# Kernel optimization log

Hardware: AMD Instinct MI355X
Metric: run time of the kernel (lower is better)

The kernel has to match this reference:

```python
import jax, jax.numpy as jnp
import numpy as np

B, D, E, C = 16384, 2048, 16, 64  # batch, feat_dim, num_experts, classes per expert
CLASS_STARTS = np.arange(E, dtype=np.int32) * C  # contiguous equal-size class ranges


def setup_inputs() -> dict:
    key = jax.random.key(0)
    k1, k2, k3, k4, k5 = jax.random.split(key, 5)
    return {
        "features": jax.random.normal(k1, (B, D), dtype=jnp.float32),
        "coarse_w": jax.random.normal(k2, (E, D), dtype=jnp.float32) * 0.02,
        "coarse_b": jax.random.normal(k3, (E,), dtype=jnp.float32) * 0.02,
        "expert_w": jax.random.normal(k4, (E, C, D), dtype=jnp.float32) * 0.02,
        "expert_b": jax.random.normal(k5, (E, C), dtype=jnp.float32) * 0.02,
    }


def reference(features, coarse_w, coarse_b, expert_w, expert_b):
    # coarse router: Linear(feat_dim -> num_experts)
    coarse_output = features @ coarse_w.T + coarse_b          # [B, E]
    expert_id = jnp.argmax(coarse_output, axis=1)             # [B] top-1 routing

    # all-expert heads as one batched GEMM, then select routed expert per sample
    # (same math as gather-by-mask + per-expert Linear + scatter-back loop)
    y_all = jnp.einsum('bd,ecd->bec', features, expert_w) + expert_b  # [B, E, C]
    y = jnp.take_along_axis(y_all, expert_id[:, None, None], axis=1)[:, 0, :]  # [B, C]

    # local_preds: softmax probs of the routed expert (all experts have C = max classes)
    local_preds = jax.nn.softmax(y, axis=1)                   # [B, C]

    # global prediction = local argmax + expert's class-range start
    starts = jnp.asarray(CLASS_STARTS)
    global_preds = (jnp.argmax(y, axis=1) + starts[expert_id]).astype(jnp.float32)  # [B]

    return coarse_output, expert_id, local_preds, global_preds
```

## Files before the change

### kernel.cpp

```cpp
#include <hip/hip_runtime.h>
#include <cstdint>

typedef _Float16 f16;
typedef f16 f16x8 __attribute__((ext_vector_type(8)));
typedef float f32x4 __attribute__((ext_vector_type(4)));
#define MFMA16(a, b, c) __builtin_amdgcn_mfma_f32_16x16x32_f16((a), (b), (c), 0, 0, 0)

static constexpr int B_ = 16384;
static constexpr int D_ = 2048;
static constexpr int E_ = 16;
static constexpr int C_ = 64;
static constexpr float LSC = 2048.0f;
static constexpr float ILSC = 1.0f / 2048.0f;
static constexpr int TR_E = 128;
static constexpr int SK_E = 8;
static constexpr int MAXITEMS = (B_ / TR_E) + E_;

__device__ __forceinline__ void cvt_hl(const float4 x, const float4 y,
                                       f16x8& h, f16x8& l) {
  const float av[8] = {x.x, x.y, x.z, x.w, y.x, y.y, y.z, y.w};
#pragma unroll
  for (int j = 0; j < 8; ++j) {
    const f16 hh = (f16)av[j];
    h[j] = hh;
    l[j] = (f16)((av[j] - (float)hh) * LSC);
  }
}

__global__ __launch_bounds__(256) void convert_w(
    const float* __restrict__ cw, const float* __restrict__ ew,
    f16* __restrict__ cwH, f16* __restrict__ cwL,
    f16* __restrict__ ewH, f16* __restrict__ ewL) {
  const int g = blockIdx.x;
  const int tid = threadIdx.x;
  const float* src;
  f16 *dh, *dl;
  size_t off;
  if (g < 16) {
    off = ((size_t)g * 256 + tid) * 8;
    src = cw; dh = cwH; dl = cwL;
  } else {
    off = ((size_t)(g - 16) * 256 + tid) * 8;
    src = ew; dh = ewH; dl = ewL;
  }
  const float4 v0 = *(const float4*)(src + off);
  const float4 v1 = *(const float4*)(src + off + 4);
  f16x8 h8, l8;
  cvt_hl(v0, v1, h8, l8);
  *(f16x8*)(dh + off) = h8;
  *(f16x8*)(dl + off) = l8;
}

__global__ __launch_bounds__(512) void coarse_fused(
    const float* __restrict__ feat, const f16* __restrict__ cwH,
    const f16* __restrict__ cwL, const float* __restrict__ cb,
    float* __restrict__ out0, float* __restrict__ out1,
    int* __restrict__ eidArr) {
  __shared__ float red[8 * 256];
  const int tid = threadIdx.x;
  const int w = tid >> 6;
  const int lane = tid & 63;
  const int rl = lane & 15;
  const int kq = lane >> 4;
  const int row = blockIdx.x * 16 + rl;
  const int k0 = w * (D_ / 8);

  const float* fr = feat + (size_t)row * D_ + k0 + kq * 8;
  const f16* bhp = cwH + (size_t)rl * D_ + k0 + kq * 8;
  const f16* blp = cwL + (size_t)rl * D_ + k0 + kq * 8;

  f32x4 aH = {0.f, 0.f, 0.f, 0.f};
  f32x4 aC = {0.f, 0.f, 0.f, 0.f};

  float4 v0 = *(const float4*)(fr);
  float4 v1 = *(const float4*)(fr + 4);
  f16x8 bhn = *(const f16x8*)(bhp);
  f16x8 bln = *(const f16x8*)(blp);
#pragma unroll
  for (int ch = 0; ch < 8; ++ch) {
    const float4 c0 = v0, c1 = v1;
    const f16x8 bh = bhn, bl = bln;
    if (ch + 1 < 8) {
      const int ko = (ch + 1) * 32;
      v0 = *(const float4*)(fr + ko);
      v1 = *(const float4*)(fr + ko + 4);
      bhn = *(const f16x8*)(bhp + ko);
      bln = *(const f16x8*)(blp + ko);
    }
    f16x8 h8, l8;
    cvt_hl(c0, c1, h8, l8);
    aH = MFMA16(h8, bh, aH);
    aC = MFMA16(h8, bl, aC);
    aC = MFMA16(l8, bh, aC);
  }
#pragma unroll
  for (int reg = 0; reg < 4; ++reg)
    red[w * 256 + (kq * 4 + reg) * 16 + rl] = aH[reg] + aC[reg] * ILSC;
  __syncthreads();

  if (tid < 256) {
    const int e = tid & 15;
    const int lrow = tid >> 4;
    float val = cb[e];
#pragma unroll
    for (int ww = 0; ww < 8; ++ww) val += red[ww * 256 + tid];
    const int grow = blockIdx.x * 16 + lrow;
    out0[(size_t)grow * E_ + e] = val;
    float av2 = val;
    int ai = e;
#pragma unroll
    for (int off = 8; off; off >>= 1) {
      const float ov = __shfl_xor(av2, off, 16);
      const int oi = __shfl_xor(ai, off, 16);
      if (ov > av2 || (ov == av2 && oi < ai)) { av2 = ov; ai = oi; }
    }
    if (e == 0) {
      out1[grow] = (float)ai;
      eidArr[grow] = ai;
    }
  }
}

__global__ __launch_bounds__(256) void route_build(
    const int* __restrict__ eidArr, int* __restrict__ cnt,
    int* __restrict__ rowList, int* __restrict__ sched,
    int* __restrict__ nItems, int* __restrict__ doneCnt) {
  __shared__ int lcnt[E_];
  __shared__ int lbase[E_];
  __shared__ int tiles[E_];
  __shared__ int offs[E_];
  __shared__ int isLast;
  const int tid = threadIdx.x;
  if (tid < E_) lcnt[tid] = 0;
  __syncthreads();
  const int row = blockIdx.x * 256 + tid;
  const int best = eidArr[row];
  const int lpos = atomicAdd(&lcnt[best], 1);
  __syncthreads();
  if (tid < E_) lbase[tid] = atomicAdd(&cnt[tid], lcnt[tid]);
  __syncthreads();
  rowList[best * B_ + lbase[best] + lpos] = row;

  __syncthreads();
  if (tid == 0) {
    __threadfence();
    const int d = atomicAdd(doneCnt, 1);
    isLast = (d == (int)gridDim.x - 1) ? 1 : 0;
  }
  __syncthreads();
  if (isLast) {
    if (tid < E_)
      tiles[tid] = (atomicAdd(&cnt[tid], 0) + TR_E - 1) / TR_E;
    __syncthreads();
    if (tid == 0) {
      int acc = 0;
      for (int e2 = 0; e2 < E_; ++e2) { offs[e2] = acc; acc += tiles[e2]; }
      *nItems = acc;
    }
    __syncthreads();
    if (tid < E_) {
      const int o = offs[tid], n = tiles[tid];
      for (int k = 0; k < n; ++k) sched[o + k] = tid | (k << 8);
    }
  }
}

__global__ __launch_bounds__(256) void expert_gemm(
    const float* __restrict__ feat,
    const f16* __restrict__ ewH, const f16* __restrict__ ewL,
    const int* __restrict__ rowList, const int* __restrict__ cnt,
    const int* __restrict__ sched, const int* __restrict__ nItems,
    float* __restrict__ part0, float* __restrict__ partRest) {
  __shared__ int rIdx[TR_E];
  const int b = blockIdx.x;
  const int kz = b % SK_E;
  const int item = b / SK_E;
  if (item >= *nItems) return;
  const int s = sched[item];
  const int e = s & 255;
  const int tile = s >> 8;
  const int count = cnt[e];

  const int tid = threadIdx.x;
  if (tid < TR_E) {
    const int slot = tile * TR_E + tid;
    rIdx[tid] = (slot < count) ? rowList[e * B_ + slot] : 0;
  }
  __syncthreads();

  const int lane = tid & 63;
  const int w = tid >> 6;
  const int rl = lane & 15;
  const int kq = lane >> 4;

  const int grow0 = rIdx[w * 32 + rl];
  const int grow1 = rIdx[w * 32 + 16 + rl];
  constexpr int KRANGE = D_ / SK_E;
  constexpr int NCH = KRANGE / 32;
  const int k0 = kz * KRANGE;

  const float* pa0 = feat + (size_t)grow0 * D_ + k0 + kq * 8;
  const float* pa1 = feat + (size_t)grow1 * D_ + k0 + kq * 8;
  const size_t eoff = (size_t)e * C_ * D_;
  const f16* pbh[4];
  const f16* pbl[4];
#pragma unroll
  for (int ct = 0; ct < 4; ++ct) {
    const size_t co = eoff + (size_t)(ct * 16 + rl) * D_ + k0 + kq * 8;
    pbh[ct] = ewH + co;
    pbl[ct] = ewL + co;
  }

  f32x4 accH[2][4], accC[2][4];
#pragma unroll
  for (int s2 = 0; s2 < 2; ++s2)
#pragma unroll
    for (int ct = 0; ct < 4; ++ct) {
      accH[s2][ct] = (f32x4){0.f, 0.f, 0.f, 0.f};
      accC[s2][ct] = (f32x4){0.f, 0.f, 0.f, 0.f};
    }

  float4 n0a = *(const float4*)(pa0);
  float4 n0b = *(const float4*)(pa0 + 4);
  float4 n1a = *(const float4*)(pa1);
  float4 n1b = *(const float4*)(pa1 + 4);
  f16x8 bhn[4], bln[4];
#pragma unroll
  for (int ct = 0; ct < 4; ++ct) {
    bhn[ct] = *(const f16x8*)(pbh[ct]);
    bln[ct] = *(const f16x8*)(pbl[ct]);
  }
#pragma unroll
  for (int ch = 0; ch < NCH; ++ch) {
    const float4 c0a = n0a, c0b = n0b, c1a = n1a, c1b = n1b;
    f16x8 bhc[4], blc[4];
#pragma unroll
    for (int ct = 0; ct < 4; ++ct) { bhc[ct] = bhn[ct]; blc[ct] = bln[ct]; }
    if (ch + 1 < NCH) {
      const int kn = (ch + 1) * 32;
      n0a = *(const float4*)(pa0 + kn);
      n0b = *(const float4*)(pa0 + kn + 4);
      n1a = *(const float4*)(pa1 + kn);
      n1b = *(const float4*)(pa1 + kn + 4);
#pragma unroll
      for (int ct = 0; ct < 4; ++ct) {
        bhn[ct] = *(const f16x8*)(pbh[ct] + kn);
        bln[ct] = *(const f16x8*)(pbl[ct] + kn);
      }
    }
    f16x8 a0h, a0l, a1h, a1l;
    cvt_hl(c0a, c0b, a0h, a0l);
    cvt_hl(c1a, c1b, a1h, a1l);
#pragma unroll
    for (int ct = 0; ct < 4; ++ct) {
      accH[0][ct] = MFMA16(a0h, bhc[ct], accH[0][ct]);
      accC[0][ct] = MFMA16(a0h, blc[ct], accC[0][ct]);
      accC[0][ct] = MFMA16(a0l, bhc[ct], accC[0][ct]);
      accH[1][ct] = MFMA16(a1h, bhc[ct], accH[1][ct]);
      accC[1][ct] = MFMA16(a1h, blc[ct], accC[1][ct]);
      accC[1][ct] = MFMA16(a1l, bhc[ct], accC[1][ct]);
    }
  }

  float* pk = kz ? (partRest + (size_t)(kz - 1) * B_ * C_) : part0;
#pragma unroll
  for (int s2 = 0; s2 < 2; ++s2)
#pragma unroll
    for (int reg = 0; reg < 4; ++reg) {
      const int rloc = w * 32 + s2 * 16 + kq * 4 + reg;
      const int slot = tile * TR_E + rloc;
      if (slot < count) {
        const int g = rIdx[rloc];
#pragma unroll
        for (int ct = 0; ct < 4; ++ct)
          pk[(size_t)g * C_ + ct * 16 + rl] =
              accH[s2][ct][reg] + accC[s2][ct][reg] * ILSC;
      }
    }
}

template <int SK>
__global__ __launch_bounds__(256) void finish_rows(
    const float* __restrict__ ypart0, const float* __restrict__ ypartRest,
    const float* __restrict__ eb, const int* __restrict__ eidArr,
    float* __restrict__ out2, float* __restrict__ out3) {
  const int lane = threadIdx.x & 63;
  const int row = (blockIdx.x * 256 + threadIdx.x) >> 6;
  const int eid = eidArr[row];

  float v = eb[eid * C_ + lane];
  v += ypart0[(size_t)row * C_ + lane];
#pragma unroll
  for (int kz = 1; kz < SK; ++kz)
    v += ypartRest[((size_t)(kz - 1) * B_ + row) * C_ + lane];

  float m = v;
#pragma unroll
  for (int off = 32; off; off >>= 1) m = fmaxf(m, __shfl_xor(m, off, 64));
  const float p = __expf(v - m);
  float s = p;
#pragma unroll
  for (int off = 32; off; off >>= 1) s += __shfl_xor(s, off, 64);
  out2[(size_t)row * C_ + lane] = p / s;

  float av = v;
  int ai = lane;
#pragma unroll
  for (int off = 32; off; off >>= 1) {
    const float ov = __shfl_xor(av, off, 64);
    const int oi = __shfl_xor(ai, off, 64);
    if (ov > av || (ov == av && oi < ai)) { av = ov; ai = oi; }
  }
  if (lane == 0) out3[row] = (float)(ai + (eid << 6));
}

extern "C" void kernel_launch(void* const* d_in, const int* in_sizes, int n_in,
                              void* d_out, int out_size, void* d_ws,
                              size_t ws_size, hipStream_t stream) {
  const float* feat = (const float*)d_in[0];
  const float* cw = (const float*)d_in[1];
  const float* cb = (const float*)d_in[2];
  const float* ew = (const float*)d_in[3];
  const float* eb = (const float*)d_in[4];

  float* out0 = (float*)d_out;
  float* out1 = out0 + (size_t)B_ * E_;
  float* out2 = out1 + B_;
  float* out3 = out2 + (size_t)B_ * C_;

  char* p = (char*)d_ws;
  f16* ewH = (f16*)p;        p += (size_t)E_ * C_ * D_ * 2;
  f16* ewL = (f16*)p;        p += (size_t)E_ * C_ * D_ * 2;
  f16* cwH = (f16*)p;        p += (size_t)E_ * D_ * 2;
  f16* cwL = (f16*)p;        p += (size_t)E_ * D_ * 2;
  float* ypartRest = (float*)p; p += (size_t)(SK_E - 1) * B_ * C_ * 4;
  int* rowList = (int*)p;    p += (size_t)E_ * B_ * 4;
  int* cnt = (int*)p;        p += 64 * 4;
  int* eidArr = (int*)p;     p += (size_t)B_ * 4;
  int* sched = (int*)p;      p += 512 * 4;
  int* nItems = (int*)p;
  int* doneCnt = cnt + 16;

  hipMemsetAsync(cnt, 0, 32 * sizeof(int), stream);

  convert_w<<<16 + 1024, 256, 0, stream>>>(cw, ew, cwH, cwL, ewH, ewL);
  coarse_fused<<<B_ / 16, 512, 0, stream>>>(feat, cwH, cwL, cb, out0, out1,
                                            eidArr);
  route_build<<<B_ / 256, 256, 0, stream>>>(eidArr, cnt, rowList, sched,
                                            nItems, doneCnt);
  expert_gemm<<<MAXITEMS * SK_E, 256, 0, stream>>>(
      feat, ewH, ewL, rowList, cnt, sched, nItems, out2, ypartRest);
  finish_rows<SK_E><<<(B_ * 64) / 256, 256, 0, stream>>>(out2, ypartRest, eb,
                                                         eidArr, out2, out3);
}
```

Baseline: 290.1 us.

## Fuse routing into coarse kernel and softmax epilogue into expert GEMM

Routing-list construction moves into the coarse kernel, so the separate route_build launch and the eidArr round trip go away. The counter memset is folded into the weight-conversion kernel. The expert GEMM changes from 128-row tiles with 8-way split-K partials to 16-row tiles with a 2-wave in-block K split. Bias, softmax and argmax now run in its epilogue, which removes the partial-sum buffers and the finish kernel. The trade-off is that each feature row and weight chunk is now reused far less per block, so weight traffic per output rises, and the blocks are small.

```diff
diff --git a/kernel.cpp b/kernel.cpp
--- a/kernel.cpp
+++ b/kernel.cpp
@@ -12,9 +12,8 @@
 static constexpr int C_ = 64;
 static constexpr float LSC = 2048.0f;
 static constexpr float ILSC = 1.0f / 2048.0f;
-static constexpr int TR_E = 128;
-static constexpr int SK_E = 8;
-static constexpr int MAXITEMS = (B_ / TR_E) + E_;
+static constexpr int TR_X = 16;
+static constexpr int MAXITEMS = B_ / TR_X + E_;
 
 __device__ __forceinline__ void cvt_hl(const float4 x, const float4 y,
                                        f16x8& h, f16x8& l) {
@@ -30,9 +29,10 @@
 __global__ __launch_bounds__(256) void convert_w(
     const float* __restrict__ cw, const float* __restrict__ ew,
     f16* __restrict__ cwH, f16* __restrict__ cwL,
-    f16* __restrict__ ewH, f16* __restrict__ ewL) {
+    f16* __restrict__ ewH, f16* __restrict__ ewL, int* __restrict__ cnt) {
   const int g = blockIdx.x;
   const int tid = threadIdx.x;
+  if (g == 0 && tid < 32) cnt[tid] = 0;
   const float* src;
   f16 *dh, *dl;
   size_t off;
@@ -55,13 +55,21 @@
     const float* __restrict__ feat, const f16* __restrict__ cwH,
     const f16* __restrict__ cwL, const float* __restrict__ cb,
     float* __restrict__ out0, float* __restrict__ out1,
-    int* __restrict__ eidArr) {
+    int* __restrict__ cnt, int* __restrict__ rowList,
+    int* __restrict__ sched, int* __restrict__ nItems,
+    int* __restrict__ doneCnt) {
   __shared__ float red[8 * 256];
+  __shared__ int lcnt[E_];
+  __shared__ int lbase[E_];
+  __shared__ int tiles[E_];
+  __shared__ int offs[E_];
+  __shared__ int isLast;
   const int tid = threadIdx.x;
   const int w = tid >> 6;
   const int lane = tid & 63;
   const int rl = lane & 15;
   const int kq = lane >> 4;
+  if (tid < E_) lcnt[tid] = 0;
   const int row = blockIdx.x * 16 + rl;
   const int k0 = w * (D_ / 8);
 
@@ -98,13 +106,14 @@
     red[w * 256 + (kq * 4 + reg) * 16 + rl] = aH[reg] + aC[reg] * ILSC;
   __syncthreads();
 
+  int best = -1, lpos = 0, grow = 0;
   if (tid < 256) {
     const int e = tid & 15;
     const int lrow = tid >> 4;
     float val = cb[e];
 #pragma unroll
     for (int ww = 0; ww < 8; ++ww) val += red[ww * 256 + tid];
-    const int grow = blockIdx.x * 16 + lrow;
+    grow = blockIdx.x * 16 + lrow;
     out0[(size_t)grow * E_ + e] = val;
     float av2 = val;
     int ai = e;
@@ -116,30 +125,14 @@
     }
     if (e == 0) {
       out1[grow] = (float)ai;
-      eidArr[grow] = ai;
-    }
-  }
-}
-
-__global__ __launch_bounds__(256) void route_build(
-    const int* __restrict__ eidArr, int* __restrict__ cnt,
-    int* __restrict__ rowList, int* __restrict__ sched,
-    int* __restrict__ nItems, int* __restrict__ doneCnt) {
-  __shared__ int lcnt[E_];
-  __shared__ int lbase[E_];
-  __shared__ int tiles[E_];
-  __shared__ int offs[E_];
-  __shared__ int isLast;
-  const int tid = threadIdx.x;
-  if (tid < E_) lcnt[tid] = 0;
-  __syncthreads();
-  const int row = blockIdx.x * 256 + tid;
-  const int best = eidArr[row];
-  const int lpos = atomicAdd(&lcnt[best], 1);
+      best = ai;
+      lpos = atomicAdd(&lcnt[ai], 1);
+    }
+  }
   __syncthreads();
   if (tid < E_) lbase[tid] = atomicAdd(&cnt[tid], lcnt[tid]);
   __syncthreads();
-  rowList[best * B_ + lbase[best] + lpos] = row;
+  if (best >= 0) rowList[best * B_ + lbase[best] + lpos] = grow;
 
   __syncthreads();
   if (tid == 0) {
@@ -150,7 +143,7 @@
   __syncthreads();
   if (isLast) {
     if (tid < E_)
-      tiles[tid] = (atomicAdd(&cnt[tid], 0) + TR_E - 1) / TR_E;
+      tiles[tid] = (atomicAdd(&cnt[tid], 0) + TR_X - 1) / TR_X;
     __syncthreads();
     if (tid == 0) {
       int acc = 0;
@@ -165,16 +158,16 @@
   }
 }
 
-__global__ __launch_bounds__(256) void expert_gemm(
+__global__ __launch_bounds__(128) void expert_fused(
     const float* __restrict__ feat,
     const f16* __restrict__ ewH, const f16* __restrict__ ewL,
-    const int* __restrict__ rowList, const int* __restrict__ cnt,
-    const int* __restrict__ sched, const int* __restrict__ nItems,
-    float* __restrict__ part0, float* __restrict__ partRest) {
-  __shared__ int rIdx[TR_E];
-  const int b = blockIdx.x;
-  const int kz = b % SK_E;
-  const int item = b / SK_E;
+    const float* __restrict__ eb, const int* __restrict__ rowList,
+    const int* __restrict__ cnt, const int* __restrict__ sched,
+    const int* __restrict__ nItems,
+    float* __restrict__ out2, float* __restrict__ out3) {
+  __shared__ int rIdx[TR_X];
+  __shared__ float yred[TR_X * C_];
+  const int item = blockIdx.x;
   if (item >= *nItems) return;
   const int s = sched[item];
   const int e = s & 255;
@@ -182,8 +175,8 @@
   const int count = cnt[e];
 
   const int tid = threadIdx.x;
-  if (tid < TR_E) {
-    const int slot = tile * TR_E + tid;
+  if (tid < TR_X) {
+    const int slot = tile * TR_X + tid;
     rIdx[tid] = (slot < count) ? rowList[e * B_ + slot] : 0;
   }
   __syncthreads();
@@ -193,14 +186,12 @@
   const int rl = lane & 15;
   const int kq = lane >> 4;
 
-  const int grow0 = rIdx[w * 32 + rl];
-  const int grow1 = rIdx[w * 32 + 16 + rl];
-  constexpr int KRANGE = D_ / SK_E;
-  constexpr int NCH = KRANGE / 32;
-  const int k0 = kz * KRANGE;
-
-  const float* pa0 = feat + (size_t)grow0 * D_ + k0 + kq * 8;
-  const float* pa1 = feat + (size_t)grow1 * D_ + k0 + kq * 8;
+  const int growA = rIdx[rl];
+  constexpr int KR = D_ / 2;
+  constexpr int NCH = KR / 32;
+  const int k0 = w * KR;
+
+  const float* pa = feat + (size_t)growA * D_ + k0 + kq * 8;
   const size_t eoff = (size_t)e * C_ * D_;
   const f16* pbh[4];
   const f16* pbl[4];
@@ -211,107 +202,93 @@
     pbl[ct] = ewL + co;
   }
 
-  f32x4 accH[2][4], accC[2][4];
-#pragma unroll
-  for (int s2 = 0; s2 < 2; ++s2)
-#pragma unroll
-    for (int ct = 0; ct < 4; ++ct) {
-      accH[s2][ct] = (f32x4){0.f, 0.f, 0.f, 0.f};
-      accC[s2][ct] = (f32x4){0.f, 0.f, 0.f, 0.f};
-    }
-
-  float4 n0a = *(const float4*)(pa0);
-  float4 n0b = *(const float4*)(pa0 + 4);
-  float4 n1a = *(const float4*)(pa1);
-  float4 n1b = *(const float4*)(pa1 + 4);
+  f32x4 accH[4], accC[4];
+#pragma unroll
+  for (int ct = 0; ct < 4; ++ct) {
+    accH[ct] = (f32x4){0.f, 0.f, 0.f, 0.f};
+    accC[ct] = (f32x4){0.f, 0.f, 0.f, 0.f};
+  }
+
+  float4 na = *(const float4*)(pa);
+  float4 nb = *(const float4*)(pa + 4);
   f16x8 bhn[4], bln[4];
 #pragma unroll
   for (int ct = 0; ct < 4; ++ct) {
     bhn[ct] = *(const f16x8*)(pbh[ct]);
     bln[ct] = *(const f16x8*)(pbl[ct]);
   }
-#pragma unroll
   for (int ch = 0; ch < NCH; ++ch) {
-    const float4 c0a = n0a, c0b = n0b, c1a = n1a, c1b = n1b;
+    const float4 ca = na, cb2 = nb;
     f16x8 bhc[4], blc[4];
 #pragma unroll
     for (int ct = 0; ct < 4; ++ct) { bhc[ct] = bhn[ct]; blc[ct] = bln[ct]; }
     if (ch + 1 < NCH) {
       const int kn = (ch + 1) * 32;
-      n0a = *(const float4*)(pa0 + kn);
-      n0b = *(const float4*)(pa0 + kn + 4);
-      n1a = *(const float4*)(pa1 + kn);
-      n1b = *(const float4*)(pa1 + kn + 4);
+      na = *(const float4*)(pa + kn);
+      nb = *(const float4*)(pa + kn + 4);
 #pragma unroll
       for (int ct = 0; ct < 4; ++ct) {
         bhn[ct] = *(const f16x8*)(pbh[ct] + kn);
         bln[ct] = *(const f16x8*)(pbl[ct] + kn);
       }
     }
-    f16x8 a0h, a0l, a1h, a1l;
-    cvt_hl(c0a, c0b, a0h, a0l);
-    cvt_hl(c1a, c1b, a1h, a1l);
+    f16x8 ah, al;
+    cvt_hl(ca, cb2, ah, al);
 #pragma unroll
     for (int ct = 0; ct < 4; ++ct) {
-      accH[0][ct] = MFMA16(a0h, bhc[ct], accH[0][ct]);
-      accC[0][ct] = MFMA16(a0h, blc[ct], accC[0][ct]);
-      accC[0][ct] = MFMA16(a0l, bhc[ct], accC[0][ct]);
-      accH[1][ct] = MFMA16(a1h, bhc[ct], accH[1][ct]);
-      accC[1][ct] = MFMA16(a1h, blc[ct], accC[1][ct]);
-      accC[1][ct] = MFMA16(a1l, bhc[ct], accC[1][ct]);
-    }
-  }
-
-  float* pk = kz ? (partRest + (size_t)(kz - 1) * B_ * C_) : part0;
-#pragma unroll
-  for (int s2 = 0; s2 < 2; ++s2)
+      accH[ct] = MFMA16(ah, bhc[ct], accH[ct]);
+      accC[ct] = MFMA16(ah, blc[ct], accC[ct]);
+      accC[ct] = MFMA16(al, bhc[ct], accC[ct]);
+    }
+  }
+
+  if (w == 1) {
+#pragma unroll
+    for (int ct = 0; ct < 4; ++ct)
+#pragma unroll
+      for (int reg = 0; reg < 4; ++reg)
+        yred[(kq * 4 + reg) * C_ + ct * 16 + rl] =
+            accH[ct][reg] + accC[ct][reg] * ILSC;
+  }
+  __syncthreads();
+  if (w == 0) {
 #pragma unroll
     for (int reg = 0; reg < 4; ++reg) {
-      const int rloc = w * 32 + s2 * 16 + kq * 4 + reg;
-      const int slot = tile * TR_E + rloc;
+      const int lrow = kq * 4 + reg;
+      float v[4];
+#pragma unroll
+      for (int ct = 0; ct < 4; ++ct)
+        v[ct] = accH[ct][reg] + accC[ct][reg] * ILSC +
+                yred[lrow * C_ + ct * 16 + rl] + eb[e * C_ + ct * 16 + rl];
+      float m = fmaxf(fmaxf(v[0], v[1]), fmaxf(v[2], v[3]));
+#pragma unroll
+      for (int off = 8; off; off >>= 1) m = fmaxf(m, __shfl_xor(m, off, 16));
+      float p[4], ssum = 0.f;
+#pragma unroll
+      for (int ct = 0; ct < 4; ++ct) { p[ct] = __expf(v[ct] - m); ssum += p[ct]; }
+#pragma unroll
+      for (int off = 8; off; off >>= 1) ssum += __shfl_xor(ssum, off, 16);
+      const int slot = tile * TR_X + lrow;
+      const int g = rIdx[lrow];
       if (slot < count) {
-        const int g = rIdx[rloc];
 #pragma unroll
         for (int ct = 0; ct < 4; ++ct)
-          pk[(size_t)g * C_ + ct * 16 + rl] =
-              accH[s2][ct][reg] + accC[s2][ct][reg] * ILSC;
+          out2[(size_t)g * C_ + ct * 16 + rl] = p[ct] / ssum;
       }
-    }
-}
-
-template <int SK>
-__global__ __launch_bounds__(256) void finish_rows(
-    const float* __restrict__ ypart0, const float* __restrict__ ypartRest,
-    const float* __restrict__ eb, const int* __restrict__ eidArr,
-    float* __restrict__ out2, float* __restrict__ out3) {
-  const int lane = threadIdx.x & 63;
-  const int row = (blockIdx.x * 256 + threadIdx.x) >> 6;
-  const int eid = eidArr[row];
-
-  float v = eb[eid * C_ + lane];
-  v += ypart0[(size_t)row * C_ + lane];
-#pragma unroll
-  for (int kz = 1; kz < SK; ++kz)
-    v += ypartRest[((size_t)(kz - 1) * B_ + row) * C_ + lane];
-
-  float m = v;
-#pragma unroll
-  for (int off = 32; off; off >>= 1) m = fmaxf(m, __shfl_xor(m, off, 64));
-  const float p = __expf(v - m);
-  float s = p;
-#pragma unroll
-  for (int off = 32; off; off >>= 1) s += __shfl_xor(s, off, 64);
-  out2[(size_t)row * C_ + lane] = p / s;
-
-  float av = v;
-  int ai = lane;
-#pragma unroll
-  for (int off = 32; off; off >>= 1) {
-    const float ov = __shfl_xor(av, off, 64);
-    const int oi = __shfl_xor(ai, off, 64);
-    if (ov > av || (ov == av && oi < ai)) { av = ov; ai = oi; }
-  }
-  if (lane == 0) out3[row] = (float)(ai + (eid << 6));
+      float av = v[0];
+      int ai = rl;
+#pragma unroll
+      for (int ct = 1; ct < 4; ++ct)
+        if (v[ct] > av) { av = v[ct]; ai = ct * 16 + rl; }
+#pragma unroll
+      for (int off = 8; off; off >>= 1) {
+        const float ov = __shfl_xor(av, off, 16);
+        const int oi = __shfl_xor(ai, off, 16);
+        if (ov > av || (ov == av && oi < ai)) { av = ov; ai = oi; }
+      }
+      if (slot < count && rl == 0) out3[g] = (float)(ai + (e << 6));
+    }
+  }
 }
 
 extern "C" void kernel_launch(void* const* d_in, const int* in_sizes, int n_in,
@@ -329,27 +306,20 @@
   float* out3 = out2 + (size_t)B_ * C_;
 
   char* p = (char*)d_ws;
-  f16* ewH = (f16*)p;        p += (size_t)E_ * C_ * D_ * 2;
-  f16* ewL = (f16*)p;        p += (size_t)E_ * C_ * D_ * 2;
-  f16* cwH = (f16*)p;        p += (size_t)E_ * D_ * 2;
-  f16* cwL = (f16*)p;        p += (size_t)E_ * D_ * 2;
-  float* ypartRest = (float*)p; p += (size_t)(SK_E - 1) * B_ * C_ * 4;
-  int* rowList = (int*)p;    p += (size_t)E_ * B_ * 4;
-  int* cnt = (int*)p;        p += 64 * 4;
-  int* eidArr = (int*)p;     p += (size_t)B_ * 4;
-  int* sched = (int*)p;      p += 512 * 4;
+  f16* ewH = (f16*)p;     p += (size_t)E_ * C_ * D_ * 2;
+  f16* ewL = (f16*)p;     p += (size_t)E_ * C_ * D_ * 2;
+  f16* cwH = (f16*)p;     p += (size_t)E_ * D_ * 2;
+  f16* cwL = (f16*)p;     p += (size_t)E_ * D_ * 2;
+  int* rowList = (int*)p; p += (size_t)E_ * B_ * 4;
+  int* cnt = (int*)p;     p += 64 * 4;
+  int* sched = (int*)p;   p += 1056 * 4;
   int* nItems = (int*)p;
   int* doneCnt = cnt + 16;
 
-  hipMemsetAsync(cnt, 0, 32 * sizeof(int), stream);
-
-  convert_w<<<16 + 1024, 256, 0, stream>>>(cw, ew, cwH, cwL, ewH, ewL);
+  convert_w<<<16 + 1024, 256, 0, stream>>>(cw, ew, cwH, cwL, ewH, ewL, cnt);
   coarse_fused<<<B_ / 16, 512, 0, stream>>>(feat, cwH, cwL, cb, out0, out1,
-                                            eidArr);
-  route_build<<<B_ / 256, 256, 0, stream>>>(eidArr, cnt, rowList, sched,
-                                            nItems, doneCnt);
-  expert_gemm<<<MAXITEMS * SK_E, 256, 0, stream>>>(
-      feat, ewH, ewL, rowList, cnt, sched, nItems, out2, ypartRest);
-  finish_rows<SK_E><<<(B_ * 64) / 256, 256, 0, stream>>>(out2, ypartRest, eb,
-                                                         eidArr, out2, out3);
-}
+                                            cnt, rowList, sched, nItems,
+                                            doneCnt);
+  expert_fused<<<MAXITEMS, 128, 0, stream>>>(feat, ewH, ewL, eb, rowList,
+                                             cnt, sched, nItems, out2, out3);
+}
```

Measured after the change: 355.1 us. 22.4% more time.
